# Kernel tuning notes

Hardware: AMD Instinct MI355X
Metric: run time of the kernel (lower is better)

Reference implementation:

```python
import jax, jax.numpy as jnp
import numpy as np

B, T, D, H = 2, 2048, 1024, 16
DH = D // H  # 64


def setup_inputs() -> dict:
    key = jax.random.key(0)
    ks = jax.random.split(key, 8)
    s = 0.02  # typical init scale for projection weights
    return {
        "query_states": jax.random.normal(ks[0], (B, T, D), jnp.float32),
        "key_states": jax.random.normal(ks[1], (B, T, D), jnp.float32),
        "attention_mask": jnp.zeros((B, 1, 1, T), jnp.float32),
        "Wq": jax.random.normal(ks[2], (D, D), jnp.float32) * s,
        "bq": jnp.zeros((D,), jnp.float32),
        "Wk": jax.random.normal(ks[3], (D, D), jnp.float32) * s,
        "bk": jnp.zeros((D,), jnp.float32),
        "Wv": jax.random.normal(ks[4], (D, D), jnp.float32) * s,
        "bv": jnp.zeros((D,), jnp.float32),
        "mask_future": 0,
    }


def _heads(x):
    # [B, T, D] -> [B, H, T, DH]
    b, t, _ = x.shape
    return x.reshape(b, t, H, DH).transpose(0, 2, 1, 3)


def reference(query_states, key_states, attention_mask, Wq, bq, Wk, bk, Wv, bv, mask_future):
    q = _heads(query_states @ Wq + bq)   # [B,H,T,DH]
    k = _heads(key_states @ Wk + bk)     # [B,H,T,DH]
    v = _heads(key_states @ Wv + bv)     # [B,H,T,DH]
    scale = 1.0 / jnp.sqrt(jnp.asarray(DH, jnp.float32))
    scores = jnp.einsum("bhqd,bhkd->bhqk", q, k) * scale + attention_mask
    if mask_future:  # static Python int flag
        t = scores.shape[-1]
        triu = jnp.triu(jnp.ones((t, t), bool))  # includes diagonal, as in torch.triu
        scores = jnp.where(triu, -jnp.inf, scores)
    probs = jax.nn.softmax(scores, axis=-1)
    # dropout p=0.0 -> identity
    ctx = jnp.einsum("bhqk,bhkd->bhqd", probs, v)  # [B,H,T,DH]
    b, _, t, _ = ctx.shape
    return ctx.transpose(0, 2, 1, 3).reshape(b, t, H * DH)
```

## Files before the change

kernel.cpp:

```cpp
#include <hip/hip_runtime.h>

#define DEV __device__ __forceinline__

typedef _Float16 f16;
typedef __attribute__((ext_vector_type(2))) _Float16 f16x2;
typedef __attribute__((ext_vector_type(4))) _Float16 f16x4;
typedef __attribute__((ext_vector_type(8))) _Float16 f16x8;
typedef __attribute__((ext_vector_type(4))) float f32x4;
typedef __attribute__((ext_vector_type(16))) float f32x16;
typedef __attribute__((ext_vector_type(4))) int i32x4;

constexpr int B = 2, T = 2048, D = 1024, H = 16, DH = 64;
constexpr int M = B * T;
constexpr float LOG2E = 1.4426950408889634f;

DEV void gload_lds16(const void* g, void* l) {
  __builtin_amdgcn_global_load_lds(
      (const __attribute__((address_space(1))) void*)g,
      (__attribute__((address_space(3))) void*)l, 16, 0, 0);
}

DEV unsigned pack_pk(float a, float b) {
  auto v = __builtin_amdgcn_cvt_pkrtz(a, b);
  return __builtin_bit_cast(unsigned, v);
}

DEV float max3f(float a, float b, float c) { return fmaxf(fmaxf(a, b), c); }

#if __has_builtin(__builtin_amdgcn_permlane32_swap)
#define HAVE_PLSWAP 1
DEV void swap32(unsigned& a, unsigned& b) {
  auto r = __builtin_amdgcn_permlane32_swap((int)a, (int)b, false, false);
  a = (unsigned)r[0];
  b = (unsigned)r[1];
}
DEV float redmax32(float x) {
  unsigned a = __builtin_bit_cast(unsigned, x), b = a;
  swap32(a, b);
  return fmaxf(__builtin_bit_cast(float, a), __builtin_bit_cast(float, b));
}
DEV float redsum32(float x) {
  unsigned a = __builtin_bit_cast(unsigned, x), b = a;
  swap32(a, b);
  return __builtin_bit_cast(float, a) + __builtin_bit_cast(float, b);
}
#else
#define HAVE_PLSWAP 0
DEV float redmax32(float x) { return fmaxf(x, __shfl_xor(x, 32, 64)); }
DEV float redsum32(float x) { return x + __shfl_xor(x, 32, 64); }
#endif

__global__ __launch_bounds__(256) void cast_f32_f16(
    const float* __restrict__ in, f16* __restrict__ out, int n) {
  int i = (blockIdx.x * 256 + threadIdx.x) * 8;
  if (i >= n) return;
  f32x4 a = *(const f32x4*)(in + i);
  f32x4 b = *(const f32x4*)(in + i + 4);
  f16x8 o;
  o[0] = (f16)a[0]; o[1] = (f16)a[1]; o[2] = (f16)a[2]; o[3] = (f16)a[3];
  o[4] = (f16)b[0]; o[5] = (f16)b[1]; o[6] = (f16)b[2]; o[7] = (f16)b[3];
  *(f16x8*)(out + i) = o;
}

__global__ __launch_bounds__(256) void transpose_cast(
    const float* __restrict__ Wq, const float* __restrict__ Wk,
    const float* __restrict__ Wv, f16* __restrict__ WT) {
  int mat = blockIdx.z;
  const float* W = (mat == 0) ? Wq : (mat == 1 ? Wk : Wv);
  f16* out = WT + (size_t)mat * D * D;
  __shared__ float tile[32][33];
  int nt = blockIdx.x * 32, kt = blockIdx.y * 32;
  int tx = threadIdx.x, ty = threadIdx.y;
  for (int j = 0; j < 4; ++j) {
    int r = ty + 8 * j;
    tile[r][tx] = W[(size_t)(kt + r) * D + nt + tx];
  }
  __syncthreads();
  for (int j = 0; j < 4; ++j) {
    int r = ty + 8 * j;
    out[(size_t)(nt + r) * D + kt + tx] = (f16)tile[tx][r];
  }
}

__global__ __launch_bounds__(256) void qkv_gemm(
    const f16* __restrict__ XQ, const f16* __restrict__ XK,
    const f16* __restrict__ WT, const float* __restrict__ bq,
    const float* __restrict__ bk, const float* __restrict__ bv,
    f16* __restrict__ QKV) {
  int mat = blockIdx.z;
  const f16* X = (mat == 0) ? XQ : XK;
  const f16* Wt = WT + (size_t)mat * D * D;
  const float* bias = (mat == 0) ? bq : (mat == 1 ? bk : bv);
  f16* out = QKV + (size_t)mat * M * D;
  float oscale = (mat == 0) ? 0.125f * LOG2E : 1.0f;
  int Lb = blockIdx.x + 8 * blockIdx.y;
  int n0 = (Lb & 7) * 128, m0 = (Lb >> 3) * 128;

  __shared__ f16 lA[128 * 64];
  __shared__ f16 lB[128 * 64];
  char* lAb = (char*)lA;
  char* lBb = (char*)lB;

  int tid = threadIdx.x;
  int w = tid >> 6, lane = tid & 63;
  int l15 = lane & 15, lhi = lane >> 4;
  int wr = w >> 1, wc = w & 1;
  int r8 = lane >> 3, slot = lane & 7;
  int sslot = slot ^ r8;

  f32x4 acc[4][4] = {};

  for (int kt = 0; kt < D / 64; ++kt) {
    __syncthreads();
    for (int i = 0; i < 4; ++i) {
      int chunk = w * 4 + i;
      int row = chunk * 8 + r8;
      const f16* srcA = X + (size_t)(m0 + row) * D + kt * 64 + sslot * 8;
      gload_lds16(srcA, lAb + chunk * 1024);
      const f16* srcB = Wt + (size_t)(n0 + row) * D + kt * 64 + sslot * 8;
      gload_lds16(srcB, lBb + chunk * 1024);
    }
    __syncthreads();
    for (int ks = 0; ks < 2; ++ks) {
      f16x8 aF[4], bF[4];
      for (int mt = 0; mt < 4; ++mt) {
        int row = wr * 64 + mt * 16 + l15;
        int byt = (row * 128 + ks * 64 + lhi * 16) ^ ((row & 7) << 4);
        aF[mt] = *(const f16x8*)(lAb + byt);
      }
      for (int nt = 0; nt < 4; ++nt) {
        int row = wc * 64 + nt * 16 + l15;
        int byt = (row * 128 + ks * 64 + lhi * 16) ^ ((row & 7) << 4);
        bF[nt] = *(const f16x8*)(lBb + byt);
      }
      for (int mt = 0; mt < 4; ++mt)
        for (int nt = 0; nt < 4; ++nt)
          acc[mt][nt] = __builtin_amdgcn_mfma_f32_16x16x32_f16(
              aF[mt], bF[nt], acc[mt][nt], 0, 0, 0);
    }
  }

  float bv4[4];
  for (int nt = 0; nt < 4; ++nt) bv4[nt] = bias[n0 + wc * 64 + nt * 16 + l15];
  if (mat < 2) {
    for (int mt = 0; mt < 4; ++mt)
      for (int nt = 0; nt < 4; ++nt) {
        int col = n0 + wc * 64 + nt * 16 + l15;
        int hh = col >> 6, dh = col & 63;
        for (int r = 0; r < 4; ++r) {
          int row = m0 + wr * 64 + mt * 16 + lhi * 4 + r;
          int bb = row >> 11, tt = row & (T - 1);
          out[((size_t)(bb * H + hh) * T + tt) * 64 + dh] =
              (f16)((acc[mt][nt][r] + bv4[nt]) * oscale);
        }
      }
  } else {
    for (int mt = 0; mt < 4; ++mt)
      for (int nt = 0; nt < 4; ++nt) {
        int col = n0 + wc * 64 + nt * 16 + l15;
        int hh = col >> 6, dh = col & 63;
        int row0 = m0 + wr * 64 + mt * 16 + lhi * 4;
        int bb = row0 >> 11, tt = row0 & (T - 1);
        f16x4 pk;
        for (int r = 0; r < 4; ++r) pk[r] = (f16)(acc[mt][nt][r] + bv4[nt]);
        *(f16x4*)(out + ((size_t)(bb * H + hh) * 64 + dh) * T + tt) = pk;
      }
  }
}

__global__ __launch_bounds__(256) void attn(
    const f16* __restrict__ QKV, const float* __restrict__ mask,
    const int* __restrict__ mfp, float* __restrict__ out) {
  int L = blockIdx.x + 16 * blockIdx.y + 256 * blockIdx.z;
  int e = L & 7, q = L >> 3;
  int bh = e * 4 + (q & 3);
  int q0 = (q >> 2) * 128;
  int b = bh >> 4, h = bh & 15;
  int mf = *mfp;
  constexpr int NT = T / 64;

  const f16* Qh = QKV + (size_t)bh * T * 64;
  const f16* Kh = QKV + (size_t)M * D + (size_t)bh * T * 64;
  const f16* VTh = QKV + (size_t)2 * M * D + (size_t)bh * 64 * T;

  __shared__ char smem[32768];

  int tid = threadIdx.x;
  int w = tid >> 6, lane = tid & 63;
  int l31 = lane & 31, hi = lane >> 5;
  int qrow = q0 + w * 32 + l31;

  const float* mb = mask + (size_t)b * T;
  bool lnz = false;
#pragma unroll
  for (int j = 0; j < 8; ++j) {
    f32x4 mv = *(const f32x4*)(mb + lane * 32 + j * 4);
    lnz |= (mv[0] != 0.f) | (mv[1] != 0.f) | (mv[2] != 0.f) | (mv[3] != 0.f);
  }
  int domask = __any(lnz) | mf;

  f16x8 qF[4];
  const f16* qp = Qh + (size_t)qrow * 64;
#pragma unroll
  for (int kc = 0; kc < 4; ++kc) qF[kc] = *(const f16x8*)(qp + kc * 16 + hi * 8);

  auto STAGE = [&](int kv0, int buf) {
    char* dK = smem + buf * 8192;
    char* dV = smem + 16384 + buf * 8192;
#pragma unroll
    for (int i = 0; i < 2; ++i) {
      int c = (w * 2 + i) * 64 + lane;
      int r = c >> 3;
      int slot = (c & 7) ^ (r & 7);
      gload_lds16(Kh + (size_t)(kv0 + r) * 64 + slot * 8, dK + (w * 2 + i) * 1024);
      gload_lds16(VTh + (size_t)r * T + kv0 + slot * 8, dV + (w * 2 + i) * 1024);
    }
  };

  float mprev = -1e30f, lsum = 0.f;
  f32x16 oAcc[2] = {};
  STAGE(0, 0);
  __syncthreads();

  for (int t = 0; t < NT; ++t) {
    if (t) __syncthreads();
    if (t + 1 < NT) STAGE((t + 1) * 64, (t + 1) & 1);
    int kv0 = t * 64;
    const char* bK = smem + (t & 1) * 8192;
    const char* bV = smem + 16384 + (t & 1) * 8192;

    f32x16 sA[2] = {};
    __builtin_amdgcn_s_setprio(1);
#pragma unroll
    for (int f = 0; f < 2; ++f)
#pragma unroll
      for (int kc = 0; kc < 4; ++kc) {
        int row = f * 32 + l31;
        f16x8 kF = *(const f16x8*)(bK + ((row * 128 + kc * 32 + hi * 16) ^ ((row & 7) << 4)));
        sA[f] = __builtin_amdgcn_mfma_f32_32x32x16_f16(kF, qF[kc], sA[f], 0, 0, 0);
      }
    __builtin_amdgcn_s_setprio(0);

    float mx;
    if (domask) {
      mx = -1e30f;
#pragma unroll
      for (int f = 0; f < 2; ++f)
#pragma unroll
        for (int r = 0; r < 16; ++r) {
          int kv = kv0 + f * 32 + (r & 3) + 8 * (r >> 2) + 4 * hi;
          float v = sA[f][r] + LOG2E * mb[kv];
          if (mf && kv >= qrow) v = -1e30f;
          sA[f][r] = v;
          mx = fmaxf(mx, v);
        }
    } else {
      float t0 = max3f(sA[0][0], sA[0][1], sA[0][2]);
      float t1 = max3f(sA[0][3], sA[0][4], sA[0][5]);
      float t2 = max3f(sA[0][6], sA[0][7], sA[0][8]);
      float t3 = max3f(sA[0][9], sA[0][10], sA[0][11]);
      float t4 = max3f(sA[0][12], sA[0][13], sA[0][14]);
      float t5 = max3f(sA[1][0], sA[1][1], sA[1][2]);
      float t6 = max3f(sA[1][3], sA[1][4], sA[1][5]);
      float t7 = max3f(sA[1][6], sA[1][7], sA[1][8]);
      float t8 = max3f(sA[1][9], sA[1][10], sA[1][11]);
      float t9 = max3f(sA[1][12], sA[1][13], sA[1][14]);
      float u0 = max3f(t0, t1, t2);
      float u1 = max3f(t3, t4, sA[0][15]);
      float u2 = max3f(t5, t6, t7);
      float u3 = max3f(t8, t9, sA[1][15]);
      mx = fmaxf(max3f(u0, u1, u2), u3);
    }
    mx = redmax32(mx);

    if (!__all(mx <= mprev + 8.f)) {
      float mn = fmaxf(mprev, mx);
      float asc = __builtin_amdgcn_exp2f(mprev - mn);
      lsum *= asc;
#pragma unroll
      for (int f = 0; f < 2; ++f)
#pragma unroll
        for (int r = 0; r < 16; ++r) oAcc[f][r] *= asc;
      mprev = mn;
    }

    float rs = 0.f;
#pragma unroll
    for (int f = 0; f < 2; ++f)
#pragma unroll
      for (int r = 0; r < 16; ++r) {
        float e2 = __builtin_amdgcn_exp2f(sA[f][r] - mprev);
        sA[f][r] = e2;
        rs += e2;
      }
    lsum += redsum32(rs);

    f16x8 pF[4];
#if HAVE_PLSWAP
#pragma unroll
    for (int f = 0; f < 2; ++f)
#pragma unroll
      for (int half = 0; half < 2; ++half) {
        unsigned p0 = pack_pk(sA[f][half * 8 + 0], sA[f][half * 8 + 1]);
        unsigned p1 = pack_pk(sA[f][half * 8 + 2], sA[f][half * 8 + 3]);
        unsigned p2 = pack_pk(sA[f][half * 8 + 4], sA[f][half * 8 + 5]);
        unsigned p3 = pack_pk(sA[f][half * 8 + 6], sA[f][half * 8 + 7]);
        swap32(p0, p2);
        swap32(p1, p3);
        i32x4 d;
        d[0] = (int)p0; d[1] = (int)p1; d[2] = (int)p2; d[3] = (int)p3;
        pF[f * 2 + half] = __builtin_bit_cast(f16x8, d);
      }
#else
#pragma unroll
    for (int f = 0; f < 2; ++f) {
      unsigned pk_[8], px_[8];
#pragma unroll
      for (int g = 0; g < 8; ++g) {
        pk_[g] = pack_pk(sA[f][2 * g], sA[f][2 * g + 1]);
        px_[g] = (unsigned)__shfl_xor((int)pk_[g], 32, 64);
      }
#pragma unroll
      for (int half = 0; half < 2; ++half) {
        int o = half * 4;
        i32x4 d;
        d[0] = (int)(hi ? px_[o + 2] : pk_[o + 0]);
        d[1] = (int)(hi ? px_[o + 3] : pk_[o + 1]);
        d[2] = (int)(hi ? pk_[o + 2] : px_[o + 0]);
        d[3] = (int)(hi ? pk_[o + 3] : px_[o + 1]);
        pF[f * 2 + half] = __builtin_bit_cast(f16x8, d);
      }
    }
#endif

    __builtin_amdgcn_s_setprio(1);
#pragma unroll
    for (int df = 0; df < 2; ++df)
#pragma unroll
      for (int kc = 0; kc < 4; ++kc) {
        int row = df * 32 + l31;
        f16x8 vF = *(const f16x8*)(bV + ((row * 128 + kc * 32 + hi * 16) ^ ((row & 7) << 4)));
        oAcc[df] = __builtin_amdgcn_mfma_f32_32x32x16_f16(vF, pF[kc], oAcc[df], 0, 0, 0);
      }
    __builtin_amdgcn_s_setprio(0);
  }

  __syncthreads();
  float linv = 1.0f / lsum;
  float* sOw = (float*)smem + w * 2048;
#pragma unroll
  for (int df = 0; df < 2; ++df)
#pragma unroll
    for (int r = 0; r < 16; ++r) {
      int d = df * 32 + 4 * hi + (r & 3) + 8 * (r >> 2);
      sOw[l31 * 64 + (d ^ l31)] = oAcc[df][r] * linv;
    }
  __syncthreads();
  float* op0 = out + (size_t)(b * T + q0 + w * 32) * D + h * 64;
#pragma unroll
  for (int r2 = 0; r2 < 32; ++r2) {
    float v = sOw[r2 * 64 + (lane ^ r2)];
    op0[(size_t)r2 * D + lane] = v;
  }
}

extern "C" void kernel_launch(void* const* d_in, const int* in_sizes, int n_in,
                              void* d_out, int out_size, void* d_ws, size_t ws_size,
                              hipStream_t stream) {
  const float* q_in = (const float*)d_in[0];
  const float* k_in = (const float*)d_in[1];
  const float* amask = (const float*)d_in[2];
  const float* Wq = (const float*)d_in[3];
  const float* bq = (const float*)d_in[4];
  const float* Wk = (const float*)d_in[5];
  const float* bk = (const float*)d_in[6];
  const float* Wv = (const float*)d_in[7];
  const float* bv = (const float*)d_in[8];
  const int* mf = (const int*)d_in[9];
  float* out = (float*)d_out;

  char* ws = (char*)d_ws;
  f16* XQ = (f16*)ws;
  f16* XK = (f16*)(ws + (((size_t)8) << 20));
  f16* WT = (f16*)(ws + (((size_t)16) << 20));
  f16* QKV = (f16*)(ws + (((size_t)24) << 20));

  cast_f32_f16<<<2048, 256, 0, stream>>>(q_in, XQ, M * D);
  cast_f32_f16<<<2048, 256, 0, stream>>>(k_in, XK, M * D);
  transpose_cast<<<dim3(32, 32, 3), dim3(32, 8), 0, stream>>>(Wq, Wk, Wv, WT);
  qkv_gemm<<<dim3(8, 32, 3), 256, 0, stream>>>(XQ, XK, WT, bq, bk, bv, QKV);
  attn<<<dim3(16, 16, 2), 256, 0, stream>>>(QKV, amask, mf, out);
}
```

Before: 214.9 us.

## Software-pipeline PV MFMA of previous tile behind QK MFMA of current tile

Restructures the attention loop so the P·V matrix multiply for tile t-1 is issued right after the Q·K multiply for tile t, letting softmax work overlap with MFMA execution. V fragments are loaded from LDS into registers at the start of each tile, before the next buffer is overwritten. The loop is manually unrolled by two with ping-pong register sets, plus a drain step after the loop. The row-sum is also changed to a tree reduction. The extra V and P register sets raise VGPR pressure and could lower occupancy.

```diff
diff --git a/kernel.cpp b/kernel.cpp
--- a/kernel.cpp
+++ b/kernel.cpp
@@ -26,6 +26,14 @@
 }
 
 DEV float max3f(float a, float b, float c) { return fmaxf(fmaxf(a, b), c); }
+
+DEV float sum16(const f32x16& v) {
+  float a = (v[0] + v[1]) + (v[2] + v[3]);
+  float b = (v[4] + v[5]) + (v[6] + v[7]);
+  float c = (v[8] + v[9]) + (v[10] + v[11]);
+  float d = (v[12] + v[13]) + (v[14] + v[15]);
+  return (a + b) + (c + d);
+}
 
 #if __has_builtin(__builtin_amdgcn_permlane32_swap)
 #define HAVE_PLSWAP 1
@@ -219,16 +227,28 @@
 
   float mprev = -1e30f, lsum = 0.f;
   f32x16 oAcc[2] = {};
+  f16x8 vA[8], vB[8], pA[4], pB[4];
+
   STAGE(0, 0);
   __syncthreads();
 
-  for (int t = 0; t < NT; ++t) {
+  auto TILE = [&](int t, f16x8 (&vCur)[8], f16x8 (&vPrev)[8],
+                  f16x8 (&pCur)[4], f16x8 (&pPrev)[4], bool doPV) {
     if (t) __syncthreads();
     if (t + 1 < NT) STAGE((t + 1) * 64, (t + 1) & 1);
     int kv0 = t * 64;
     const char* bK = smem + (t & 1) * 8192;
     const char* bV = smem + 16384 + (t & 1) * 8192;
 
+#pragma unroll
+    for (int df = 0; df < 2; ++df)
+#pragma unroll
+      for (int kc = 0; kc < 4; ++kc) {
+        int row = df * 32 + l31;
+        vCur[df * 4 + kc] =
+            *(const f16x8*)(bV + ((row * 128 + kc * 32 + hi * 16) ^ ((row & 7) << 4)));
+      }
+
     f32x16 sA[2] = {};
     __builtin_amdgcn_s_setprio(1);
 #pragma unroll
@@ -236,9 +256,18 @@
 #pragma unroll
       for (int kc = 0; kc < 4; ++kc) {
         int row = f * 32 + l31;
-        f16x8 kF = *(const f16x8*)(bK + ((row * 128 + kc * 32 + hi * 16) ^ ((row & 7) << 4)));
+        f16x8 kF =
+            *(const f16x8*)(bK + ((row * 128 + kc * 32 + hi * 16) ^ ((row & 7) << 4)));
         sA[f] = __builtin_amdgcn_mfma_f32_32x32x16_f16(kF, qF[kc], sA[f], 0, 0, 0);
       }
+    if (doPV) {
+#pragma unroll
+      for (int df = 0; df < 2; ++df)
+#pragma unroll
+        for (int kc = 0; kc < 4; ++kc)
+          oAcc[df] = __builtin_amdgcn_mfma_f32_32x32x16_f16(
+              vPrev[df * 4 + kc], pPrev[kc], oAcc[df], 0, 0, 0);
+    }
     __builtin_amdgcn_s_setprio(0);
 
     float mx;
@@ -284,18 +313,13 @@
       mprev = mn;
     }
 
-    float rs = 0.f;
 #pragma unroll
     for (int f = 0; f < 2; ++f)
 #pragma unroll
-      for (int r = 0; r < 16; ++r) {
-        float e2 = __builtin_amdgcn_exp2f(sA[f][r] - mprev);
-        sA[f][r] = e2;
-        rs += e2;
-      }
-    lsum += redsum32(rs);
-
-    f16x8 pF[4];
+      for (int r = 0; r < 16; ++r)
+        sA[f][r] = __builtin_amdgcn_exp2f(sA[f][r] - mprev);
+    lsum += redsum32(sum16(sA[0]) + sum16(sA[1]));
+
 #if HAVE_PLSWAP
 #pragma unroll
     for (int f = 0; f < 2; ++f)
@@ -309,7 +333,7 @@
         swap32(p1, p3);
         i32x4 d;
         d[0] = (int)p0; d[1] = (int)p1; d[2] = (int)p2; d[3] = (int)p3;
-        pF[f * 2 + half] = __builtin_bit_cast(f16x8, d);
+        pCur[f * 2 + half] = __builtin_bit_cast(f16x8, d);
       }
 #else
 #pragma unroll
@@ -328,22 +352,27 @@
         d[1] = (int)(hi ? px_[o + 3] : pk_[o + 1]);
         d[2] = (int)(hi ? pk_[o + 2] : px_[o + 0]);
         d[3] = (int)(hi ? pk_[o + 3] : px_[o + 1]);
-        pF[f * 2 + half] = __builtin_bit_cast(f16x8, d);
+        pCur[f * 2 + half] = __builtin_bit_cast(f16x8, d);
       }
     }
 #endif
-
-    __builtin_amdgcn_s_setprio(1);
-#pragma unroll
-    for (int df = 0; df < 2; ++df)
-#pragma unroll
-      for (int kc = 0; kc < 4; ++kc) {
-        int row = df * 32 + l31;
-        f16x8 vF = *(const f16x8*)(bV + ((row * 128 + kc * 32 + hi * 16) ^ ((row & 7) << 4)));
-        oAcc[df] = __builtin_amdgcn_mfma_f32_32x32x16_f16(vF, pF[kc], oAcc[df], 0, 0, 0);
-      }
-    __builtin_amdgcn_s_setprio(0);
-  }
+  };
+
+  TILE(0, vA, vB, pA, pB, false);
+  for (int t = 1; t + 1 < NT; t += 2) {
+    TILE(t, vB, vA, pB, pA, true);
+    TILE(t + 1, vA, vB, pA, pB, true);
+  }
+  TILE(NT - 1, vB, vA, pB, pA, true);
+
+  __builtin_amdgcn_s_setprio(1);
+#pragma unroll
+  for (int df = 0; df < 2; ++df)
+#pragma unroll
+    for (int kc = 0; kc < 4; ++kc)
+      oAcc[df] = __builtin_amdgcn_mfma_f32_32x32x16_f16(vB[df * 4 + kc], pB[kc],
+                                                        oAcc[df], 0, 0, 0);
+  __builtin_amdgcn_s_setprio(0);
 
   __syncthreads();
   float linv = 1.0f / lsum;
```

Result: slower. 219.6 us (+2.2%).

## Double-buffer QKV GEMM LDS tiles and merge the Q/K cast kernels

Applied to the files above, without the earlier changes.

The QKV GEMM now keeps two LDS buffers, so the async global-to-LDS loads for the next K-tile are issued before the MFMA work on the current tile. That removes one barrier per iteration and lets memory latency overlap with compute. The MFMA block is wrapped in s_setprio to raise wave priority, and the inner loops are explicitly unrolled. The two f32-to-f16 cast launches are merged into one kernel writing a contiguous buffer. The trade-off is that LDS per block doubles to 64KB, which may reduce occupancy.

```diff
diff --git a/kernel.cpp b/kernel.cpp
--- a/kernel.cpp
+++ b/kernel.cpp
@@ -50,10 +50,13 @@
 DEV float redsum32(float x) { return x + __shfl_xor(x, 32, 64); }
 #endif
 
-__global__ __launch_bounds__(256) void cast_f32_f16(
-    const float* __restrict__ in, f16* __restrict__ out, int n) {
-  int i = (blockIdx.x * 256 + threadIdx.x) * 8;
-  if (i >= n) return;
+__global__ __launch_bounds__(256) void cast_qk(
+    const float* __restrict__ qin, const float* __restrict__ kin,
+    f16* __restrict__ outq) {
+  int bi = blockIdx.x;
+  const float* in = (bi < 2048) ? qin : kin;
+  f16* out = outq + ((bi < 2048) ? 0 : (size_t)M * D);
+  int i = ((bi & 2047) * 256 + threadIdx.x) * 8;
   f32x4 a = *(const f32x4*)(in + i);
   f32x4 b = *(const f32x4*)(in + i + 4);
   f16x8 o;
@@ -96,10 +99,9 @@
   int Lb = blockIdx.x + 8 * blockIdx.y;
   int n0 = (Lb & 7) * 128, m0 = (Lb >> 3) * 128;
 
-  __shared__ f16 lA[128 * 64];
-  __shared__ f16 lB[128 * 64];
-  char* lAb = (char*)lA;
-  char* lBb = (char*)lB;
+  __shared__ f16 lds[2 * 2 * 128 * 64];
+  char* lAb = (char*)lds;
+  char* lBb = (char*)lds + 16384;
 
   int tid = threadIdx.x;
   int w = tid >> 6, lane = tid & 63;
@@ -109,34 +111,51 @@
   int sslot = slot ^ r8;
 
   f32x4 acc[4][4] = {};
-
-  for (int kt = 0; kt < D / 64; ++kt) {
-    __syncthreads();
+  constexpr int NKT = D / 64;
+
+  auto STAGE = [&](int kt, int buf) {
+#pragma unroll
     for (int i = 0; i < 4; ++i) {
       int chunk = w * 4 + i;
       int row = chunk * 8 + r8;
-      const f16* srcA = X + (size_t)(m0 + row) * D + kt * 64 + sslot * 8;
-      gload_lds16(srcA, lAb + chunk * 1024);
-      const f16* srcB = Wt + (size_t)(n0 + row) * D + kt * 64 + sslot * 8;
-      gload_lds16(srcB, lBb + chunk * 1024);
-    }
-    __syncthreads();
+      gload_lds16(X + (size_t)(m0 + row) * D + kt * 64 + sslot * 8,
+                  lAb + buf * 32768 + chunk * 1024);
+      gload_lds16(Wt + (size_t)(n0 + row) * D + kt * 64 + sslot * 8,
+                  lBb + buf * 32768 + chunk * 1024);
+    }
+  };
+
+  STAGE(0, 0);
+  __syncthreads();
+
+  for (int kt = 0; kt < NKT; ++kt) {
+    if (kt) __syncthreads();
+    if (kt + 1 < NKT) STAGE(kt + 1, (kt + 1) & 1);
+    const char* bA = lAb + (kt & 1) * 32768;
+    const char* bB = lBb + (kt & 1) * 32768;
+#pragma unroll
     for (int ks = 0; ks < 2; ++ks) {
       f16x8 aF[4], bF[4];
+#pragma unroll
       for (int mt = 0; mt < 4; ++mt) {
         int row = wr * 64 + mt * 16 + l15;
         int byt = (row * 128 + ks * 64 + lhi * 16) ^ ((row & 7) << 4);
-        aF[mt] = *(const f16x8*)(lAb + byt);
-      }
+        aF[mt] = *(const f16x8*)(bA + byt);
+      }
+#pragma unroll
       for (int nt = 0; nt < 4; ++nt) {
         int row = wc * 64 + nt * 16 + l15;
         int byt = (row * 128 + ks * 64 + lhi * 16) ^ ((row & 7) << 4);
-        bF[nt] = *(const f16x8*)(lBb + byt);
-      }
+        bF[nt] = *(const f16x8*)(bB + byt);
+      }
+      __builtin_amdgcn_s_setprio(1);
+#pragma unroll
       for (int mt = 0; mt < 4; ++mt)
+#pragma unroll
         for (int nt = 0; nt < 4; ++nt)
           acc[mt][nt] = __builtin_amdgcn_mfma_f32_16x16x32_f16(
               aF[mt], bF[nt], acc[mt][nt], 0, 0, 0);
+      __builtin_amdgcn_s_setprio(0);
     }
   }
 
@@ -380,14 +399,13 @@
   float* out = (float*)d_out;
 
   char* ws = (char*)d_ws;
-  f16* XQ = (f16*)ws;
-  f16* XK = (f16*)(ws + (((size_t)8) << 20));
+  f16* XQK = (f16*)ws;
   f16* WT = (f16*)(ws + (((size_t)16) << 20));
   f16* QKV = (f16*)(ws + (((size_t)24) << 20));
 
-  cast_f32_f16<<<2048, 256, 0, stream>>>(q_in, XQ, M * D);
-  cast_f32_f16<<<2048, 256, 0, stream>>>(k_in, XK, M * D);
+  cast_qk<<<4096, 256, 0, stream>>>(q_in, k_in, XQK);
   transpose_cast<<<dim3(32, 32, 3), dim3(32, 8), 0, stream>>>(Wq, Wk, Wv, WT);
-  qkv_gemm<<<dim3(8, 32, 3), 256, 0, stream>>>(XQ, XK, WT, bq, bk, bv, QKV);
+  qkv_gemm<<<dim3(8, 32, 3), 256, 0, stream>>>(XQK, XQK + (size_t)M * D, WT, bq,
+                                               bk, bv, QKV);
   attn<<<dim3(16, 16, 2), 256, 0, stream>>>(QKV, amask, mf, out);
 }
```

New measurement: 203.5 us. 5.3% less time.
